# Kernel tuning notes

Measured on AMD Instinct MI355X. Metric: run time of the kernel, lower is better.

The kernel has to match this reference:

```python
import jax, jax.numpy as jnp
import numpy as np

B, L, E, H = 8, 1024, 1024, 16
A = E // H  # head dim 64
SCALE = A ** -0.5
NEG = jnp.finfo(jnp.float32).min


def setup_inputs() -> dict:
    key = jax.random.key(0)
    k1, k2, k3, k4, k5 = jax.random.split(key, 5)
    embeddings = jax.random.normal(k1, (B, L, E), dtype=jnp.float32)
    attn_mask = jax.random.randint(k2, (B, H, L, L), 0, 2) == 1
    attn_bias = jax.random.normal(k3, (B, H, L, L), dtype=jnp.float32)
    W_qkv = jax.random.normal(k4, (3 * E, E), dtype=jnp.float32) * (E ** -0.5)
    W_out = jax.random.normal(k5, (E, E), dtype=jnp.float32) * (E ** -0.5)
    return {"embeddings": embeddings, "attn_mask": attn_mask,
            "attn_bias": attn_bias, "W_qkv": W_qkv, "W_out": W_out}


def reference(embeddings, attn_mask, attn_bias, W_qkv, W_out):
    # fused QKV projection: torch Linear -> x @ W.T
    qkv = embeddings @ W_qkv.T                      # [B, L, 3E]
    qkv = qkv.reshape(B, L, H, 3 * A).transpose(0, 2, 1, 3)  # [B, H, L, 3A]
    q, k, v = jnp.split(qkv, 3, axis=-1)            # each [B, H, L, A]
    attn = jnp.einsum('bhqa,bhka->bhqk', q, k) * SCALE
    attn = attn + attn_bias
    attn = jnp.where(attn_mask, NEG, attn)
    attn = jax.nn.softmax(attn, axis=-1)
    values = jnp.einsum('bhqk,bhka->bhqa', attn, v)  # [B, H, L, A]
    values = values.transpose(0, 2, 1, 3).reshape(B, L, E)
    return values @ W_out.T
```

## Files before the change

### kernel.cpp

```cpp
#include <hip/hip_runtime.h>
#include <cstdint>
#include <cstddef>


typedef __bf16 bf16;
typedef __attribute__((ext_vector_type(8))) __bf16 bf16x8;
typedef __attribute__((ext_vector_type(4))) __bf16 bf16x4;
typedef __attribute__((ext_vector_type(4))) float f32x4;
typedef __attribute__((ext_vector_type(4))) int i32x4;

#define MFMA_BF16(a, b, c) __builtin_amdgcn_mfma_f32_16x16x32_bf16(a, b, c, 0, 0, 0)

static constexpr float SCALE_ = 0.125f;
static constexpr float NEGF  = -3.4028234663852886e38f;

__device__ __forceinline__ void gload_lds16(const bf16* g, bf16* l) {
  __builtin_amdgcn_global_load_lds((const __attribute__((address_space(1))) void*)g,
                                   (__attribute__((address_space(3))) void*)l,
                                   16, 0, 0);
}

__device__ __forceinline__ bf16x8 cvt8(const float* p) {
  f32x4 a = *(const f32x4*)p;
  f32x4 b = *(const f32x4*)(p + 4);
  bf16x8 r = {(bf16)a[0], (bf16)a[1], (bf16)a[2], (bf16)a[3],
              (bf16)b[0], (bf16)b[1], (bf16)b[2], (bf16)b[3]};
  return r;
}

__global__ __launch_bounds__(256) void k_qkv(const float* __restrict__ X,
                                             const float* __restrict__ W,
                                             bf16* __restrict__ Q,
                                             bf16* __restrict__ Kc,
                                             bf16* __restrict__ Vt) {
  constexpr int K = 1024;
  __shared__ __align__(16) bf16 As[128 * 64];
  __shared__ __align__(16) bf16 Bs[128 * 64];
  const int t = threadIdx.x;
  const int lane = t & 63, w = t >> 6;
  const int wr = w >> 1, wc = w & 1;
  const int li = lane & 15, g = lane >> 4;
  const int m0 = (blockIdx.x & 63) * 128;
  const int n0 = (blockIdx.x >> 6) * 128;

  f32x4 acc[4][4] = {};

  for (int kt = 0; kt < K; kt += 64) {
#pragma unroll
    for (int it = 0; it < 4; ++it) {
      int c = it * 256 + t;
      int row = c >> 3, col = (c & 7) << 3;
      *(bf16x8*)(As + c * 8) = cvt8(X + (size_t)(m0 + row) * K + kt + col);
      *(bf16x8*)(Bs + c * 8) = cvt8(W + (size_t)(n0 + row) * K + kt + col);
    }
    __syncthreads();
#pragma unroll
    for (int kk = 0; kk < 2; ++kk) {
      bf16x8 af[4], bfr[4];
#pragma unroll
      for (int i = 0; i < 4; ++i)
        af[i] = *(const bf16x8*)(As + (wr * 64 + i * 16 + li) * 64 + kk * 32 + g * 8);
#pragma unroll
      for (int j = 0; j < 4; ++j)
        bfr[j] = *(const bf16x8*)(Bs + (wc * 64 + j * 16 + li) * 64 + kk * 32 + g * 8);
#pragma unroll
      for (int i = 0; i < 4; ++i)
#pragma unroll
        for (int j = 0; j < 4; ++j)
          acc[i][j] = MFMA_BF16(af[i], bfr[j], acc[i][j]);
    }
    __syncthreads();
  }

#pragma unroll
  for (int i = 0; i < 4; ++i) {
#pragma unroll
    for (int j = 0; j < 4; ++j) {
      int col = n0 + wc * 64 + j * 16 + li;
      int h = col / 192, r = col % 192;
#pragma unroll
      for (int rg = 0; rg < 4; ++rg) {
        int row = m0 + wr * 64 + i * 16 + g * 4 + rg;
        int b = row >> 10, l = row & 1023;
        bf16 v = (bf16)acc[i][j][rg];
        if (r < 64)
          Q[((size_t)((b * 16 + h) * 1024 + l)) * 64 + r] = v;
        else if (r < 128)
          Kc[((size_t)((b * 16 + h) * 1024 + l)) * 64 + (r - 64)] = v;
        else
          Vt[((size_t)((b * 16 + h) * 64 + (r - 128))) * 1024 + l] = v;
      }
    }
  }
}

__global__ __launch_bounds__(256) void k_attn(const bf16* __restrict__ Q,
                                              const bf16* __restrict__ Kc,
                                              const bf16* __restrict__ Vt,
                                              const float* __restrict__ bias,
                                              const int* __restrict__ mask,
                                              bf16* __restrict__ Vals) {
  __shared__ __align__(16) bf16 Plds[4][2][16][80];
  const int t = threadIdx.x, lane = t & 63, w = t >> 6;
  const int li = lane & 15, g = lane >> 4;
  const int lid = blockIdx.x;
  const int bh = lid & 127;
  const int qt = lid >> 7;
  const int b = bh >> 4, h = bh & 15;
  const int q0 = qt * 64 + w * 16;

  const bf16* Qbase = Q + ((size_t)bh << 10) * 64;
  const bf16* Kbase = Kc + ((size_t)bh << 10) * 64;
  const bf16* Vbase = Vt + ((size_t)bh << 6) * 1024;
  const float* brow = bias + ((size_t)bh << 20) + (size_t)(q0 + li) * 1024 + g * 4;
  const int*   mrow = mask + ((size_t)bh << 20) + (size_t)(q0 + li) * 1024 + g * 4;

  bf16x8 qf[2];
#pragma unroll
  for (int c = 0; c < 2; ++c)
    qf[c] = *(const bf16x8*)(Qbase + (size_t)(q0 + li) * 64 + c * 32 + g * 8);

  f32x4 oacc[4] = {};
  float mrun = NEGF;
  float lrun = 0.f;

  for (int kt6 = 0; kt6 < 16; ++kt6) {
    const int kkt = kt6 * 64;
    const int par = kt6 & 1;

    f32x4 b4[4];
    i32x4 m4[4];
#pragma unroll
    for (int kkf = 0; kkf < 4; ++kkf) {
      b4[kkf] = *(const f32x4*)(brow + kkt + kkf * 16);
      m4[kkf] = *(const i32x4*)(mrow + kkt + kkf * 16);
    }

    f32x4 s[4];
#pragma unroll
    for (int kkf = 0; kkf < 4; ++kkf) {
      f32x4 ss = {0.f, 0.f, 0.f, 0.f};
#pragma unroll
      for (int c = 0; c < 2; ++c) {
        bf16x8 kf = *(const bf16x8*)(Kbase + (size_t)(kkt + kkf * 16 + li) * 64 + c * 32 + g * 8);
        ss = MFMA_BF16(kf, qf[c], ss);
      }
      s[kkf] = ss;
    }

    float tmax = NEGF;
#pragma unroll
    for (int kkf = 0; kkf < 4; ++kkf) {
#pragma unroll
      for (int rg = 0; rg < 4; ++rg) {
        float sv = s[kkf][rg] * SCALE_ + b4[kkf][rg];
        sv = m4[kkf][rg] ? NEGF : sv;
        s[kkf][rg] = sv;
        tmax = fmaxf(tmax, sv);
      }
    }
    tmax = fmaxf(tmax, __shfl_xor(tmax, 16));
    tmax = fmaxf(tmax, __shfl_xor(tmax, 32));

    float mnew = fmaxf(mrun, tmax);
    float corr = __expf(mrun - mnew);
    float psum = 0.f;

#pragma unroll
    for (int kkf = 0; kkf < 4; ++kkf) {
      float p0 = __expf(s[kkf][0] - mnew);
      float p1 = __expf(s[kkf][1] - mnew);
      float p2 = __expf(s[kkf][2] - mnew);
      float p3 = __expf(s[kkf][3] - mnew);
      psum += (p0 + p1) + (p2 + p3);
      bf16x4 pk = {(bf16)p0, (bf16)p1, (bf16)p2, (bf16)p3};
      *(bf16x4*)(&Plds[w][par][li][kkf * 16 + g * 4]) = pk;
    }
    psum += __shfl_xor(psum, 16);
    psum += __shfl_xor(psum, 32);
    lrun = lrun * corr + psum;
    mrun = mnew;

    float cq[4];
#pragma unroll
    for (int rg = 0; rg < 4; ++rg) cq[rg] = __shfl(corr, g * 4 + rg);
#pragma unroll
    for (int af = 0; af < 4; ++af)
#pragma unroll
      for (int rg = 0; rg < 4; ++rg) oacc[af][rg] *= cq[rg];

    asm volatile("s_waitcnt lgkmcnt(0)" ::: "memory");
    __builtin_amdgcn_sched_barrier(0);

#pragma unroll
    for (int c = 0; c < 2; ++c) {
      bf16x8 pf = *(const bf16x8*)(&Plds[w][par][li][c * 32 + g * 8]);
#pragma unroll
      for (int af = 0; af < 4; ++af) {
        bf16x8 vf = *(const bf16x8*)(Vbase + (size_t)(af * 16 + li) * 1024 + kkt + c * 32 + g * 8);
        oacc[af] = MFMA_BF16(pf, vf, oacc[af]);
      }
    }
  }

  float linv[4];
#pragma unroll
  for (int rg = 0; rg < 4; ++rg) linv[rg] = 1.0f / __shfl(lrun, g * 4 + rg);
#pragma unroll
  for (int af = 0; af < 4; ++af) {
#pragma unroll
    for (int rg = 0; rg < 4; ++rg) {
      int q = q0 + g * 4 + rg;
      int col = h * 64 + af * 16 + li;
      Vals[(((size_t)(b * 1024 + q)) << 10) + col] = (bf16)(oacc[af][rg] * linv[rg]);
    }
  }
}

__global__ __launch_bounds__(256) void k_out(const bf16* __restrict__ X,
                                             const float* __restrict__ W,
                                             float* __restrict__ Out) {
  constexpr int K = 1024;
  __shared__ __align__(16) bf16 As[128 * 64];
  __shared__ __align__(16) bf16 Bs[128 * 64];
  const int t = threadIdx.x;
  const int lane = t & 63, w = t >> 6;
  const int wr = w >> 1, wc = w & 1;
  const int li = lane & 15, g = lane >> 4;
  const int m0 = (blockIdx.x & 63) * 128;
  const int n0 = (blockIdx.x >> 6) * 128;

  f32x4 acc[4][4] = {};

  for (int kt = 0; kt < K; kt += 64) {
#pragma unroll
    for (int it = 0; it < 4; ++it) {
      int c = it * 256 + t;
      int row = c >> 3, col = (c & 7) << 3;
      gload_lds16(X + (size_t)(m0 + row) * K + kt + col, As + c * 8);
      *(bf16x8*)(Bs + c * 8) = cvt8(W + (size_t)(n0 + row) * K + kt + col);
    }
    __syncthreads();
#pragma unroll
    for (int kk = 0; kk < 2; ++kk) {
      bf16x8 af[4], bfr[4];
#pragma unroll
      for (int i = 0; i < 4; ++i)
        af[i] = *(const bf16x8*)(As + (wr * 64 + i * 16 + li) * 64 + kk * 32 + g * 8);
#pragma unroll
      for (int j = 0; j < 4; ++j)
        bfr[j] = *(const bf16x8*)(Bs + (wc * 64 + j * 16 + li) * 64 + kk * 32 + g * 8);
#pragma unroll
      for (int i = 0; i < 4; ++i)
#pragma unroll
        for (int j = 0; j < 4; ++j)
          acc[i][j] = MFMA_BF16(af[i], bfr[j], acc[i][j]);
    }
    __syncthreads();
  }

#pragma unroll
  for (int i = 0; i < 4; ++i) {
#pragma unroll
    for (int j = 0; j < 4; ++j) {
      int col = n0 + wc * 64 + j * 16 + li;
#pragma unroll
      for (int rg = 0; rg < 4; ++rg) {
        int row = m0 + wr * 64 + i * 16 + g * 4 + rg;
        Out[((size_t)row << 10) + col] = acc[i][j][rg];
      }
    }
  }
}

extern "C" void kernel_launch(void* const* d_in, const int* in_sizes, int n_in,
                              void* d_out, int out_size, void* d_ws, size_t ws_size,
                              hipStream_t stream) {
  const float* emb  = (const float*)d_in[0];
  const int*   mask = (const int*)d_in[1];
  const float* bias = (const float*)d_in[2];
  const float* Wqkv = (const float*)d_in[3];
  const float* Wout = (const float*)d_in[4];
  float* out = (float*)d_out;

  const size_t HEADS_ELEMS = (size_t)8 * 16 * 1024 * 64;
  bf16* Q    = (bf16*)d_ws;
  bf16* Kc   = Q + HEADS_ELEMS;
  bf16* Vt   = Kc + HEADS_ELEMS;
  bf16* Vals = Vt + HEADS_ELEMS;

  k_qkv<<<dim3(64 * 24), 256, 0, stream>>>(emb, Wqkv, Q, Kc, Vt);
  k_attn<<<dim3(2048), 256, 0, stream>>>(Q, Kc, Vt, bias, mask, Vals);
  k_out<<<dim3(64 * 8), 256, 0, stream>>>(Vals, Wout, out);
}
```

Before: 553.8 us.

## Prefetch next bias/mask tile in registers and fold mask into bias

Bias and mask loads for the next 64-key tile are issued one iteration ahead into registers, so their global-memory latency overlaps the current tile's QK MFMAs and softmax. The mask is merged into the bias before the scores are ready, which turns the score update into a single fma. The P staging buffer's row padding goes from 80 to 72 elements, and the P stores are split into two bf16x2 writes. The explicit lgkmcnt wait and sched_barrier are removed, which raises register pressure and leaves LDS ordering to the compiler.

```diff
diff --git a/kernel.cpp b/kernel.cpp
--- a/kernel.cpp
+++ b/kernel.cpp
@@ -5,7 +5,7 @@
 
 typedef __bf16 bf16;
 typedef __attribute__((ext_vector_type(8))) __bf16 bf16x8;
-typedef __attribute__((ext_vector_type(4))) __bf16 bf16x4;
+typedef __attribute__((ext_vector_type(2))) __bf16 bf16x2;
 typedef __attribute__((ext_vector_type(4))) float f32x4;
 typedef __attribute__((ext_vector_type(4))) int i32x4;
 
@@ -100,7 +100,7 @@
                                               const float* __restrict__ bias,
                                               const int* __restrict__ mask,
                                               bf16* __restrict__ Vals) {
-  __shared__ __align__(16) bf16 Plds[4][2][16][80];
+  __shared__ __align__(16) bf16 Plds[4][2][16][72];
   const int t = threadIdx.x, lane = t & 63, w = t >> 6;
   const int li = lane & 15, g = lane >> 4;
   const int lid = blockIdx.x;
@@ -124,16 +124,31 @@
   float mrun = NEGF;
   float lrun = 0.f;
 
+  f32x4 b4[4];
+  i32x4 m4[4];
+#pragma unroll
+  for (int kkf = 0; kkf < 4; ++kkf) {
+    b4[kkf] = *(const f32x4*)(brow + kkf * 16);
+    m4[kkf] = *(const i32x4*)(mrow + kkf * 16);
+  }
+
   for (int kt6 = 0; kt6 < 16; ++kt6) {
     const int kkt = kt6 * 64;
     const int par = kt6 & 1;
 
-    f32x4 b4[4];
-    i32x4 m4[4];
-#pragma unroll
-    for (int kkf = 0; kkf < 4; ++kkf) {
-      b4[kkf] = *(const f32x4*)(brow + kkt + kkf * 16);
-      m4[kkf] = *(const i32x4*)(mrow + kkt + kkf * 16);
+    f32x4 c4[4];
+#pragma unroll
+    for (int kkf = 0; kkf < 4; ++kkf)
+#pragma unroll
+      for (int rg = 0; rg < 4; ++rg)
+        c4[kkf][rg] = m4[kkf][rg] ? NEGF : b4[kkf][rg];
+
+    if (kt6 < 15) {
+#pragma unroll
+      for (int kkf = 0; kkf < 4; ++kkf) {
+        b4[kkf] = *(const f32x4*)(brow + kkt + 64 + kkf * 16);
+        m4[kkf] = *(const i32x4*)(mrow + kkt + 64 + kkf * 16);
+      }
     }
 
     f32x4 s[4];
@@ -153,8 +168,7 @@
     for (int kkf = 0; kkf < 4; ++kkf) {
 #pragma unroll
       for (int rg = 0; rg < 4; ++rg) {
-        float sv = s[kkf][rg] * SCALE_ + b4[kkf][rg];
-        sv = m4[kkf][rg] ? NEGF : sv;
+        float sv = __builtin_fmaf(s[kkf][rg], SCALE_, c4[kkf][rg]);
         s[kkf][rg] = sv;
         tmax = fmaxf(tmax, sv);
       }
@@ -173,8 +187,10 @@
       float p2 = __expf(s[kkf][2] - mnew);
       float p3 = __expf(s[kkf][3] - mnew);
       psum += (p0 + p1) + (p2 + p3);
-      bf16x4 pk = {(bf16)p0, (bf16)p1, (bf16)p2, (bf16)p3};
-      *(bf16x4*)(&Plds[w][par][li][kkf * 16 + g * 4]) = pk;
+      bf16x2 pa = {(bf16)p0, (bf16)p1};
+      bf16x2 pb = {(bf16)p2, (bf16)p3};
+      *(bf16x2*)(&Plds[w][par][li][kkf * 16 + g * 4])     = pa;
+      *(bf16x2*)(&Plds[w][par][li][kkf * 16 + g * 4 + 2]) = pb;
     }
     psum += __shfl_xor(psum, 16);
     psum += __shfl_xor(psum, 32);
@@ -188,9 +204,6 @@
     for (int af = 0; af < 4; ++af)
 #pragma unroll
       for (int rg = 0; rg < 4; ++rg) oacc[af][rg] *= cq[rg];
-
-    asm volatile("s_waitcnt lgkmcnt(0)" ::: "memory");
-    __builtin_amdgcn_sched_barrier(0);
 
 #pragma unroll
     for (int c = 0; c < 2; ++c) {
```

Result: faster. 529.0 us (-4.5%).
